# Optimization experiments

Hardware: AMD Instinct MI355X
Metric: run time of the kernel (lower is better)

The kernel has to match this reference:

```python
import jax, jax.numpy as jnp
import numpy as np
from jax import lax

MSIZE = 64
NREG = 9
POOL_W = 256


def conv2d(x, w, b, stride):
    y = lax.conv_general_dilated(x, w, (stride, stride), ((1, 1), (1, 1)),
                                 dimension_numbers=('NCHW', 'OIHW', 'NCHW'))
    return y + b[None, :, None, None]


def resize_nearest(m, h, w):
    # nearest-neighbor resize of a 2D integer mask (matches cv2 INTER_NEAREST floor mapping)
    H, W = m.shape
    ri = (np.arange(h) * H) // h
    ci = (np.arange(w) * W) // w
    return m[ri][:, ci]


def adaptive_max_1d(x, out_size):
    # x: (c, N) -> (c, out_size), torch AdaptiveMaxPool semantics along last dim
    N = x.shape[1]
    j = np.arange(out_size)
    starts = (j * N) // out_size
    ends = -((-(j + 1) * N) // out_size)  # ceil((j+1)*N/out)
    maxlen = int((ends - starts).max())
    idx = starts[:, None] + np.arange(maxlen)[None, :]  # (out, maxlen)
    valid = idx < ends[:, None]
    idx = np.minimum(idx, N - 1)
    g = x[:, idx]  # (c, out, maxlen)
    g = jnp.where(valid[None, :, :], g, -jnp.inf)
    return g.max(axis=2)


def image_cnn(x, masks_np, w1, b1, w2, b2, w3, b3, fcw, fcb):
    f = jax.nn.relu(conv2d(x, w1, b1, 2))
    f = jax.nn.relu(conv2d(f, w2, b2, 2))
    f = conv2d(f, w3, b3, 2)
    _, c, h, w = f.shape
    ff = f.reshape(c, h * w)
    mats = {}
    for i in range(NREG):
        m = resize_nearest(masks_np[i, 0], h, w).reshape(-1)
        if int((m == 1).sum()) >= 10:
            idx = np.nonzero(m == 1)[0]
            pooled = adaptive_max_1d(ff[:, idx], POOL_W)  # (16, 256)
            mats[i] = fcw @ pooled.reshape(-1) + fcb      # (MSIZE*MSIZE,)
    return mats


def mul_forward(cF, sF, content, style, cmasks_np, smasks_np,
                compress_w, compress_b, unzip_w, unzip_b, sp, cp):
    sb, sc, sh, sw = sF.shape
    X = jnp.einsum('oc,bchw->bohw', compress_w, cF) + compress_b[None, :, None, None]
    cb, cc, ch, cw = X.shape
    X = X.reshape(cc, ch * cw)
    X = X - X.mean(axis=1, keepdims=True)
    sM = image_cnn(style, smasks_np, *sp)
    cM = image_cnn(content, cmasks_np, *cp)
    sFF = sF.reshape(sc, sh * sw)
    trans = X
    fmean = jnp.zeros((sc, ch * cw), dtype=cF.dtype)
    for i in range(NREG):
        cm = resize_nearest(cmasks_np[i, 0], ch, cw).reshape(-1)
        sm = resize_nearest(smasks_np[i, 0], sh, sw).reshape(-1)
        if int((cm == 1).sum()) >= 10 and int((sm == 1).sum()) >= 10 and i in sM and i in cM:
            fgc = np.nonzero(cm == 1)[0]
            fgs = np.nonzero(sm == 1)[0]
            sMean = sFF[:, fgs].mean(axis=1, keepdims=True)            # (sc, 1)
            T = sM[i].reshape(MSIZE, MSIZE) @ cM[i].reshape(MSIZE, MSIZE)
            trans = trans.at[:, fgc].set(T @ X[:, fgc])                 # gather-mm-scatter
            fmean = fmean.at[:, fgc].set(jnp.broadcast_to(sMean, (sc, fgc.size)))
    out = jnp.einsum('oc,bchw->bohw', unzip_w, trans.reshape(cb, cc, ch, cw)) \
          + unzip_b[None, :, None, None]
    return out + fmean.reshape(out.shape)


def setup_inputs():
    key = jax.random.key(0)
    ks = jax.random.split(key, 32)
    p = lambda k, s: jax.random.normal(k, s, dtype=jnp.float32) * 0.05
    inp = {}
    inp['cF'] = jax.random.normal(ks[0], (1, 256, 256, 256), dtype=jnp.float32)
    inp['sF'] = jax.random.normal(ks[1], (1, 256, 256, 256), dtype=jnp.float32)
    inp['content'] = jax.random.normal(ks[2], (1, 3, 1024, 1024), dtype=jnp.float32)
    inp['style'] = jax.random.normal(ks[3], (1, 3, 1024, 1024), dtype=jnp.float32)
    inp['cmasks'] = jax.random.randint(ks[4], (9, 1, 256, 256), 0, 2, dtype=jnp.int32)
    inp['smasks'] = jax.random.randint(ks[5], (9, 1, 256, 256), 0, 2, dtype=jnp.int32)
    inp['compress_w'] = p(ks[6], (MSIZE, 256))
    inp['compress_b'] = p(ks[7], (MSIZE,))
    inp['unzip_w'] = p(ks[8], (256, MSIZE))
    inp['unzip_b'] = p(ks[9], (256,))
    for pre, off in (('s', 10), ('c', 20)):
        inp[pre + '_w1'] = p(ks[off + 0], (64, 3, 3, 3))
        inp[pre + '_b1'] = p(ks[off + 1], (64,))
        inp[pre + '_w2'] = p(ks[off + 2], (32, 64, 3, 3))
        inp[pre + '_b2'] = p(ks[off + 3], (32,))
        inp[pre + '_w3'] = p(ks[off + 4], (16, 32, 3, 3))
        inp[pre + '_b3'] = p(ks[off + 5], (16,))
        inp[pre + '_fcw'] = p(ks[off + 6], (MSIZE * MSIZE, 16 * POOL_W))
        inp[pre + '_fcb'] = p(ks[off + 7], (MSIZE * MSIZE,))
    return inp


def reference(cF, sF, content, style, cmasks, smasks,
              compress_w, compress_b, unzip_w, unzip_b,
              s_w1, s_b1, s_w2, s_b2, s_w3, s_b3, s_fcw, s_fcb,
              c_w1, c_b1, c_w2, c_b2, c_w3, c_b3, c_fcw, c_fcb):
    cm_np = np.asarray(cmasks)
    sm_np = np.asarray(smasks)
    sp = (s_w1, s_b1, s_w2, s_b2, s_w3, s_b3, s_fcw, s_fcb)
    cp = (c_w1, c_b1, c_w2, c_b2, c_w3, c_b3, c_fcw, c_fcb)
    return mul_forward(cF, sF, content, style, cm_np, sm_np,
                       compress_w, compress_b, unzip_w, unzip_b, sp, cp)
```

## Files before the change

### kernel.cpp

```cpp
#include <hip/hip_runtime.h>
#include <math.h>

#define TPB 256
constexpr int YC_STRIDE = 68096;

constexpr size_t OFF_COUNTS   = 0x000000;
constexpr size_t OFF_ACTIVE   = 0x000100;
constexpr size_t OFF_LCNT     = 0x000140;
constexpr size_t OFF_RBASE    = 0x000180;
constexpr size_t OFF_MUSUM    = 0x000200;
constexpr size_t OFF_MU       = 0x000400;
constexpr size_t OFF_SSUM     = 0x000800;
constexpr size_t OFF_SMEAN    = 0x00A000;
constexpr size_t OFF_W1T      = 0x00D000;
constexpr size_t OFF_W3T      = 0x00F000;
constexpr size_t OFF_W2T      = 0x014000;
constexpr size_t OFF_CWT      = 0x028000;
constexpr size_t OFF_POOLED   = 0x040000;
constexpr size_t OFF_M        = 0x090000;
constexpr size_t OFF_P        = 0x0E0000;
constexpr size_t OFF_U        = 0x180000;
constexpr size_t OFF_V        = 0x228000;
constexpr size_t OFF_CBITS    = 0x230000;
constexpr size_t OFF_SBITS    = 0x270000;
constexpr size_t OFF_CBITS128 = 0x2B0000;
constexpr size_t OFF_SBITS128 = 0x2C0000;
constexpr size_t OFF_IDX      = 0x2D0000;
constexpr size_t OFF_BC       = 0x3F8000;
constexpr size_t OFF_BBASE    = 0x400000;
constexpr size_t OFF_RLIST    = 0x410000;
constexpr size_t OFF_INV      = 0x460000;
constexpr size_t OFF_XCT      = 0x700000;
constexpr size_t OFF_F1       = 0x1700000;
constexpr size_t OFF_F2       = 0x5700000;
constexpr size_t OFF_F3       = 0x5F00000;
constexpr size_t OFF_YC       = OFF_F1;

__global__ void init_k(int* p, int n) {
    for (int i = blockIdx.x * TPB + threadIdx.x; i < n; i += gridDim.x * TPB) p[i] = 0;
}

__global__ void bits_k(const int* __restrict__ cm, const int* __restrict__ sm,
                       int* __restrict__ cbits, int* __restrict__ sbits, int* __restrict__ counts) {
    int p = blockIdx.x * TPB + threadIdx.x;
    int cb = 0, sb = 0;
#pragma unroll
    for (int r = 0; r < 9; ++r) {
        cb |= (cm[r * 65536 + p] == 1) << r;
        sb |= (sm[r * 65536 + p] == 1) << r;
    }
    cbits[p] = cb; sbits[p] = sb;
    int lane = threadIdx.x & 63;
#pragma unroll
    for (int r = 0; r < 9; ++r) {
        unsigned long long b1 = __ballot((cb >> r) & 1);
        if (lane == 0) atomicAdd(&counts[0 + r], __popcll(b1));
        unsigned long long b2 = __ballot((sb >> r) & 1);
        if (lane == 0) atomicAdd(&counts[16 + r], __popcll(b2));
    }
}

__global__ void bits128_k(const int* __restrict__ cm, const int* __restrict__ sm,
                          int* __restrict__ cbits128, int* __restrict__ sbits128, int* __restrict__ counts) {
    int p = blockIdx.x * TPB + threadIdx.x;
    int y = p >> 7, x = p & 127;
    int src = (2 * y) * 256 + 2 * x;
    int cb = 0, sb = 0;
#pragma unroll
    for (int r = 0; r < 9; ++r) {
        cb |= (cm[r * 65536 + src] == 1) << r;
        sb |= (sm[r * 65536 + src] == 1) << r;
    }
    cbits128[p] = cb; sbits128[p] = sb;
    int lane = threadIdx.x & 63;
#pragma unroll
    for (int r = 0; r < 9; ++r) {
        unsigned long long b1 = __ballot((cb >> r) & 1);
        if (lane == 0) atomicAdd(&counts[32 + r], __popcll(b1));
        unsigned long long b2 = __ballot((sb >> r) & 1);
        if (lane == 0) atomicAdd(&counts[48 + r], __popcll(b2));
    }
}

__global__ void compact_k(const int* __restrict__ sbits128, const int* __restrict__ cbits128,
                          int* __restrict__ idxlist) {
    int r = blockIdx.x, side = blockIdx.y;
    const int* bits = side ? cbits128 : sbits128;
    int* outp = idxlist + (side * 9 + r) * 16384;
    __shared__ int wcnt[4];
    __shared__ int base_s;
    int t = threadIdx.x, w = t >> 6, lane = t & 63;
    if (t == 0) base_s = 0;
    __syncthreads();
    for (int chunk = 0; chunk < 64; ++chunk) {
        int pid = chunk * 256 + t;
        int flag = (bits[pid] >> r) & 1;
        unsigned long long m = __ballot(flag);
        if (lane == 0) wcnt[w] = __popcll(m);
        __syncthreads();
        int base = base_s;
        int woff = 0;
        for (int w2 = 0; w2 < w; ++w2) woff += wcnt[w2];
        if (flag) outp[base + woff + __popcll(m & ((1ull << lane) - 1ull))] = pid;
        __syncthreads();
        if (t == 0) base_s = base + wcnt[0] + wcnt[1] + wcnt[2] + wcnt[3];
    }
}

__global__ void wtr_k(const float* __restrict__ w, float* __restrict__ wT, int OC, int ICK) {
    int i = blockIdx.x * TPB + threadIdx.x;
    int n = OC * ICK;
    if (i < n) {
        int oc = i / ICK;
        int t = i - oc * ICK;
        wT[t * OC + oc] = w[i];
    }
}

__global__ void smean_k(const float* __restrict__ sF, const int* __restrict__ sbits,
                        float* __restrict__ ssump) {
    int c = blockIdx.x;
    int pg = blockIdx.y;
    int t = threadIdx.x;
    float acc[9];
#pragma unroll
    for (int r = 0; r < 9; ++r) acc[r] = 0.f;
    int p0 = pg * 16384;
    for (int p = p0 + t; p < p0 + 16384; p += TPB) {
        float v = sF[c * 65536 + p];
        int b = sbits[p];
#pragma unroll
        for (int r = 0; r < 9; ++r)
            if (b & (1 << r)) acc[r] += v;
    }
    __shared__ float red[9 * TPB];
#pragma unroll
    for (int r = 0; r < 9; ++r) red[r * TPB + t] = acc[r];
    __syncthreads();
    for (int off = TPB / 2; off > 0; off >>= 1) {
        if (t < off)
#pragma unroll
            for (int r = 0; r < 9; ++r) red[r * TPB + t] += red[r * TPB + t + off];
        __syncthreads();
    }
    if (t < 9) ssump[(pg * 9 + t) * 256 + c] = red[t * TPB];
}

__global__ void finalize_k(const int* __restrict__ counts, int* __restrict__ activemask,
                           const float* __restrict__ ssump, float* __restrict__ sMeanArr) {
    __shared__ int am;
    if (threadIdx.x == 0) am = 0;
    __syncthreads();
    if (threadIdx.x < 9) {
        int r = threadIdx.x;
        if (counts[0 + r] >= 10 && counts[16 + r] >= 10 && counts[32 + r] >= 10 && counts[48 + r] >= 10)
            atomicOr(&am, 1 << r);
    }
    __syncthreads();
    if (threadIdx.x == 0) *activemask = am;
    for (int e = threadIdx.x; e < 2560; e += TPB) {
        int r = e >> 8, c = e & 255;
        float v = 0.f;
        if (r < 9 && ((am >> r) & 1)) {
            float s = ssump[(0 * 9 + r) * 256 + c] + ssump[(1 * 9 + r) * 256 + c]
                    + ssump[(2 * 9 + r) * 256 + c] + ssump[(3 * 9 + r) * 256 + c];
            v = s / (float)counts[16 + r];
        }
        sMeanArr[e] = v;
    }
}

__global__ void hist_k(const int* __restrict__ cbits, const int* __restrict__ activemask,
                       int* __restrict__ rmap, int* __restrict__ bc) {
    int b = blockIdx.x, t = threadIdx.x;
    int p = b * 256 + t;
    int am = *activemask;
    int bits = cbits[p] & am;
    int r = bits ? (31 - __clz(bits)) : 9;
    rmap[p] = r;
    __shared__ int wc[4][10];
    int w = t >> 6, lane = t & 63;
#pragma unroll
    for (int rr = 0; rr < 10; ++rr) {
        unsigned long long m = __ballot(r == rr);
        if (lane == rr) wc[w][rr] = __popcll(m);
    }
    __syncthreads();
    if (t < 10) bc[b * 10 + t] = wc[0][t] + wc[1][t] + wc[2][t] + wc[3][t];
}

__global__ void scan_k(const int* __restrict__ bc, int* __restrict__ bbase,
                       int* __restrict__ lcnt, int* __restrict__ rbase) {
    __shared__ int tot[10], Bs[16];
    int t = threadIdx.x;
    if (t < 10) {
        int s = 0;
        for (int b = 0; b < 256; ++b) s += bc[b * 10 + t];
        tot[t] = s;
    }
    __syncthreads();
    if (t == 0) {
        int run = 0;
        for (int r = 0; r < 10; ++r) { Bs[r] = run; run += (tot[r] + 255) & ~255; }
    }
    __syncthreads();
    if (t < 10) {
        lcnt[t] = tot[t];
        rbase[t] = Bs[t];
        int run = Bs[t];
        for (int b = 0; b < 256; ++b) { bbase[b * 10 + t] = run; run += bc[b * 10 + t]; }
    }
}

__global__ void rank_k(const int* __restrict__ rmap, const int* __restrict__ bbase,
                       int* __restrict__ inv, int* __restrict__ rlist) {
    int b = blockIdx.x, t = threadIdx.x;
    int p = b * 256 + t;
    int r = rmap[p];
    __shared__ int wc[4][10];
    int w = t >> 6, lane = t & 63;
    int prefix = 0;
#pragma unroll
    for (int rr = 0; rr < 10; ++rr) {
        unsigned long long m = __ballot(r == rr);
        if (rr == r) prefix = __popcll(m & ((1ull << lane) - 1ull));
        if (lane == rr) wc[w][rr] = __popcll(m);
    }
    __syncthreads();
    int woff = 0;
    for (int w2 = 0; w2 < w; ++w2) woff += wc[w2][r];
    int g = bbase[b * 10 + r] + woff + prefix;
    inv[p] = g;
    rlist[g] = p;
}

__global__ void conv1_k(const float* __restrict__ in, const float* __restrict__ wT,
                        const float* __restrict__ b, float* __restrict__ out) {
    int oy = blockIdx.x >> 1;
    int X0 = (blockIdx.x & 1) << 8;
    int og = blockIdx.y;
    int t = threadIdx.x;
    __shared__ float ev[3][3][260];
    __shared__ float od[3][3][264];
    for (int u = t; u < 1152; u += 256) {
        int ic = u / 384;
        int rem = u - ic * 384;
        int row = rem >> 7, q = rem & 127;
        int iy = 2 * oy - 1 + row;
        float4 v = make_float4(0.f, 0.f, 0.f, 0.f);
        if ((unsigned)iy < 1024u)
            v = *(const float4*)(in + ic * 1048576 + iy * 1024 + 2 * X0 + 4 * q);
        ev[ic][row][2 * q]     = v.x;
        od[ic][row][2 * q + 1] = v.y;
        ev[ic][row][2 * q + 1] = v.z;
        od[ic][row][2 * q + 2] = v.w;
    }
    if (t < 9) {
        int ic = t / 3, row = t % 3;
        int iy = 2 * oy - 1 + row;
        int ix = 2 * X0 - 1;
        float v = 0.f;
        if ((unsigned)iy < 1024u && ix >= 0) v = in[ic * 1048576 + iy * 1024 + ix];
        od[ic][row][0] = v;
    }
    __syncthreads();
    float acc[32];
#pragma unroll
    for (int oc = 0; oc < 32; ++oc) acc[oc] = b[og * 32 + oc];
#pragma unroll
    for (int ic = 0; ic < 3; ++ic)
#pragma unroll
        for (int ky = 0; ky < 3; ++ky) {
            float v0 = od[ic][ky][t];
            float v1 = ev[ic][ky][t];
            float v2 = od[ic][ky][t + 1];
#pragma unroll
            for (int kx = 0; kx < 3; ++kx) {
                float v = kx == 0 ? v0 : (kx == 1 ? v1 : v2);
                const float4* wp = (const float4*)(wT + (ic * 9 + ky * 3 + kx) * 64 + og * 32);
#pragma unroll
                for (int q = 0; q < 8; ++q) {
                    float4 w4 = wp[q];
                    acc[q * 4 + 0] = fmaf(w4.x, v, acc[q * 4 + 0]);
                    acc[q * 4 + 1] = fmaf(w4.y, v, acc[q * 4 + 1]);
                    acc[q * 4 + 2] = fmaf(w4.z, v, acc[q * 4 + 2]);
                    acc[q * 4 + 3] = fmaf(w4.w, v, acc[q * 4 + 3]);
                }
            }
        }
    int idx = oy * 512 + X0 + t;
#pragma unroll
    for (int oc = 0; oc < 32; ++oc) out[(og * 32 + oc) * 262144 + idx] = fmaxf(acc[oc], 0.f);
}

__global__ void f2init_k(const float* __restrict__ b, float* __restrict__ F2) {
    int idx = blockIdx.x * TPB + threadIdx.x;
#pragma unroll
    for (int oc = 0; oc < 32; ++oc) F2[oc * 65536 + idx] = b[oc];
}

__device__ __forceinline__ void c2_load(const float* __restrict__ base, int oy, int t,
                                        float4& r0, float4& r1) {
    int row0 = t >> 7, q0 = t & 127;
    int iy0 = 2 * oy - 1 + row0;
    r0 = make_float4(0.f, 0.f, 0.f, 0.f);
    if ((unsigned)iy0 < 512u) r0 = *(const float4*)(base + iy0 * 512 + 4 * q0);
    r1 = make_float4(0.f, 0.f, 0.f, 0.f);
    if (t < 128) {
        int iy1 = 2 * oy + 1;
        r1 = *(const float4*)(base + iy1 * 512 + 4 * t);
    }
}

__device__ __forceinline__ void c2_store(float (*ev)[260], float (*od)[264], int t,
                                         float4 r0, float4 r1) {
    int row0 = t >> 7, q0 = t & 127;
    ev[row0][2 * q0]     = r0.x;
    od[row0][2 * q0 + 1] = r0.y;
    ev[row0][2 * q0 + 1] = r0.z;
    od[row0][2 * q0 + 2] = r0.w;
    if (t < 128) {
        ev[2][2 * t]     = r1.x;
        od[2][2 * t + 1] = r1.y;
        ev[2][2 * t + 1] = r1.z;
        od[2][2 * t + 2] = r1.w;
    }
}

__device__ __forceinline__ void c2_compute(const float* __restrict__ wT, int ic,
                                           const float (*ev)[260], const float (*od)[264],
                                           int t, float* acc) {
#pragma unroll
    for (int ky = 0; ky < 3; ++ky) {
        float v0 = od[ky][t];
        float v1 = ev[ky][t];
        float v2 = od[ky][t + 1];
#pragma unroll
        for (int kx = 0; kx < 3; ++kx) {
            float v = kx == 0 ? v0 : (kx == 1 ? v1 : v2);
            const float4* wp = (const float4*)(wT + (ic * 9 + ky * 3 + kx) * 32);
#pragma unroll
            for (int q = 0; q < 8; ++q) {
                float4 w4 = wp[q];
                acc[q * 4 + 0] = fmaf(w4.x, v, acc[q * 4 + 0]);
                acc[q * 4 + 1] = fmaf(w4.y, v, acc[q * 4 + 1]);
                acc[q * 4 + 2] = fmaf(w4.z, v, acc[q * 4 + 2]);
                acc[q * 4 + 3] = fmaf(w4.w, v, acc[q * 4 + 3]);
            }
        }
    }
}

__global__ void conv2p_k(const float* __restrict__ in, const float* __restrict__ wT,
                         float* __restrict__ F2) {
    int oy = blockIdx.x;
    int icg = blockIdx.y;
    int t = threadIdx.x;
    __shared__ float ev[2][3][260];
    __shared__ float od[2][3][264];
    if (t < 6) od[t / 3][t % 3][0] = 0.f;
    float acc[32];
#pragma unroll
    for (int oc = 0; oc < 32; ++oc) acc[oc] = 0.f;
    int ic0 = icg * 16;
    float4 r0, r1;
    c2_load(in + ic0 * 262144, oy, t, r0, r1);
    c2_store(ev[0], od[0], t, r0, r1);
    __syncthreads();
#pragma unroll 1
    for (int i = 0; i < 16; i += 2) {
        c2_load(in + (ic0 + i + 1) * 262144, oy, t, r0, r1);
        c2_compute(wT, ic0 + i, ev[0], od[0], t, acc);
        c2_store(ev[1], od[1], t, r0, r1);
        __syncthreads();
        if (i + 2 < 16) c2_load(in + (ic0 + i + 2) * 262144, oy, t, r0, r1);
        c2_compute(wT, ic0 + i + 1, ev[1], od[1], t, acc);
        if (i + 2 < 16) c2_store(ev[0], od[0], t, r0, r1);
        __syncthreads();
    }
    int idx = oy * 256 + t;
#pragma unroll
    for (int oc = 0; oc < 32; ++oc) atomicAdd(&F2[oc * 65536 + idx], acc[oc]);
}

__global__ void relu2_k(float* __restrict__ F2) {
    int i = blockIdx.x * TPB + threadIdx.x;
    float4* p = (float4*)F2;
    float4 v = p[i];
    v.x = fmaxf(v.x, 0.f); v.y = fmaxf(v.y, 0.f);
    v.z = fmaxf(v.z, 0.f); v.w = fmaxf(v.w, 0.f);
    p[i] = v;
}

__global__ void f3init_k(const float* __restrict__ b, float* __restrict__ F3) {
    int idx = blockIdx.x * TPB + threadIdx.x;
#pragma unroll
    for (int oc = 0; oc < 16; ++oc) F3[oc * 16384 + idx] = b[oc];
}

__global__ void conv3p_k(const float* __restrict__ in, const float* __restrict__ wT,
                         float* __restrict__ F3) {
    int idx = blockIdx.x * TPB + threadIdx.x;
    int icg = blockIdx.y;
    int ox = idx & 127, oy = idx >> 7;
    float acc[16];
#pragma unroll
    for (int oc = 0; oc < 16; ++oc) acc[oc] = 0.f;
    for (int ic = icg * 8; ic < icg * 8 + 8; ++ic) {
        const float* base = in + ic * 65536;
#pragma unroll
        for (int ky = 0; ky < 3; ++ky) {
            int iy = 2 * oy - 1 + ky;
            if ((unsigned)iy < 256u)
#pragma unroll
                for (int kx = 0; kx < 3; ++kx) {
                    int ix = 2 * ox - 1 + kx;
                    if ((unsigned)ix < 256u) {
                        float v = base[iy * 256 + ix];
                        const float4* wp = (const float4*)(wT + (ic * 9 + ky * 3 + kx) * 16);
#pragma unroll
                        for (int q = 0; q < 4; ++q) {
                            float4 w4 = wp[q];
                            acc[q * 4 + 0] = fmaf(w4.x, v, acc[q * 4 + 0]);
                            acc[q * 4 + 1] = fmaf(w4.y, v, acc[q * 4 + 1]);
                            acc[q * 4 + 2] = fmaf(w4.z, v, acc[q * 4 + 2]);
                            acc[q * 4 + 3] = fmaf(w4.w, v, acc[q * 4 + 3]);
                        }
                    }
                }
        }
    }
#pragma unroll
    for (int oc = 0; oc < 16; ++oc) atomicAdd(&F3[oc * 16384 + idx], acc[oc]);
}

__global__ void pool_k(const float* __restrict__ f3, const int* __restrict__ idxbase,
                       const int* __restrict__ cnt, float* __restrict__ pooled) {
    int r = blockIdx.x >> 4;
    int c = blockIdx.x & 15;
    int j = threadIdx.x;
    int n = cnt[r];
    float m = 0.f;
    if (n >= 1) {
        int start = (j * n) >> 8;
        int end = ((j + 1) * n + 255) >> 8;
        const int* il = idxbase + r * 16384;
        m = -__builtin_inff();
        for (int t = start; t < end; ++t) m = fmaxf(m, f3[c * 16384 + il[t]]);
    }
    pooled[(r * 16 + c) * 256 + j] = m;
}

__global__ void fc_k(const float* __restrict__ fcw_s, const float* __restrict__ fcb_s,
                     const float* __restrict__ fcw_c, const float* __restrict__ fcb_c,
                     const float* __restrict__ pooled, float* __restrict__ Mout) {
    int row = blockIdx.x;
    int side = blockIdx.y;
    const float* fcw = side ? fcw_c : fcw_s;
    const float* fcb = side ? fcb_c : fcb_s;
    const float* P = pooled + side * 9 * 4096;
    int t = threadIdx.x;
    float acc[9];
#pragma unroll
    for (int r = 0; r < 9; ++r) acc[r] = 0.f;
    for (int k = t; k < 4096; k += TPB) {
        float w = fcw[row * 4096 + k];
#pragma unroll
        for (int r = 0; r < 9; ++r) acc[r] = fmaf(w, P[r * 4096 + k], acc[r]);
    }
    __shared__ float red[9 * TPB];
#pragma unroll
    for (int r = 0; r < 9; ++r) red[r * TPB + t] = acc[r];
    __syncthreads();
    for (int off = TPB / 2; off > 0; off >>= 1) {
        if (t < off)
#pragma unroll
            for (int r = 0; r < 9; ++r) red[r * TPB + t] += red[r * TPB + t + off];
        __syncthreads();
    }
    if (t < 9) Mout[(side * 9 + t) * 4096 + row] = red[t * TPB] + fcb[row];
}

__global__ void xgemm_k(const float* __restrict__ cF, const float* __restrict__ cwT,
                        float* __restrict__ XcT) {
    int p = blockIdx.x * TPB + threadIdx.x;
    int m0 = blockIdx.y * 16;
    float acc[16];
#pragma unroll
    for (int m = 0; m < 16; ++m) acc[m] = 0.f;
    for (int k0 = 0; k0 < 256; k0 += 4) {
        float xv[4];
#pragma unroll
        for (int i = 0; i < 4; ++i) xv[i] = cF[(k0 + i) * 65536 + p];
#pragma unroll
        for (int i = 0; i < 4; ++i) {
            const float4* wp = (const float4*)(cwT + (k0 + i) * 64 + m0);
#pragma unroll
            for (int q = 0; q < 4; ++q) {
                float4 w4 = wp[q];
                acc[q * 4 + 0] = fmaf(w4.x, xv[i], acc[q * 4 + 0]);
                acc[q * 4 + 1] = fmaf(w4.y, xv[i], acc[q * 4 + 1]);
                acc[q * 4 + 2] = fmaf(w4.z, xv[i], acc[q * 4 + 2]);
                acc[q * 4 + 3] = fmaf(w4.w, xv[i], acc[q * 4 + 3]);
            }
        }
    }
    float4* op = (float4*)(XcT + p * 64 + m0);
#pragma unroll
    for (int q = 0; q < 4; ++q)
        op[q] = make_float4(acc[q * 4 + 0], acc[q * 4 + 1], acc[q * 4 + 2], acc[q * 4 + 3]);
}

__global__ void muacc_k(const float* __restrict__ XcT, float* __restrict__ musum) {
    int t = threadIdx.x;
    int m = t & 63, sub = t >> 6;
    int p0 = blockIdx.x * 256;
    float a = 0.f;
    for (int i = 0; i < 64; ++i) a += XcT[(p0 + sub + i * 4) * 64 + m];
    __shared__ float red[TPB];
    red[t] = a;
    __syncthreads();
    if (t < 64) atomicAdd(&musum[t], red[t] + red[t + 64] + red[t + 128] + red[t + 192]);
}

__global__ void mufin_k(const float* __restrict__ musum, float* __restrict__ mu) {
    int t = threadIdx.x;
    if (t < 64) mu[t] = musum[t] * (1.f / 65536.f);
}

__global__ void uprep1_k(const float* __restrict__ uw, const float* __restrict__ M,
                         float* __restrict__ P) {
    int idx = blockIdx.x * TPB + threadIdx.x;
    int r = idx / 16384;
    int rem = idx & 16383;
    int c = rem >> 6, k = rem & 63;
    float a = 0.f;
#pragma unroll 8
    for (int i = 0; i < 64; ++i) a = fmaf(uw[c * 64 + i], M[r * 4096 + i * 64 + k], a);
    P[idx] = a;
}

__global__ void uprep2_k(const float* __restrict__ uw, const float* __restrict__ M,
                         const float* __restrict__ P, float* __restrict__ U) {
    int idx = blockIdx.x * TPB + threadIdx.x;
    int r = idx / 16384;
    int rem = idx & 16383;
    int c = rem >> 6, j = rem & 63;
    if (r == 9) { U[idx] = uw[c * 64 + j]; return; }
    float a = 0.f;
#pragma unroll 8
    for (int k = 0; k < 64; ++k) a = fmaf(P[r * 16384 + c * 64 + k], M[(9 + r) * 4096 + k * 64 + j], a);
    U[idx] = a;
}

__global__ void uprep3_k(const float* __restrict__ U, const float* __restrict__ mu,
                         const float* __restrict__ uzb, const float* __restrict__ sMeanArr,
                         float* __restrict__ V) {
    int r = blockIdx.x;
    int c = threadIdx.x;
    float a = uzb[c] + sMeanArr[r * 256 + c];
#pragma unroll 8
    for (int j = 0; j < 64; ++j) a -= U[r * 16384 + c * 64 + j] * mu[j];
    V[r * 256 + c] = a;
}

__global__ void ygemm_k(const float* __restrict__ XcT, const float* __restrict__ U,
                        const float* __restrict__ V, const int* __restrict__ lcnt,
                        const int* __restrict__ rbase, const int* __restrict__ rlist,
                        float* __restrict__ Yc) {
    int r = blockIdx.x >> 8;
    int c = blockIdx.x & 255;
    int ocg = blockIdx.y;
    int n = lcnt[r];
    int start = c * 256;
    if (start >= n) return;
    int i = start + threadIdx.x;
    bool valid = i < n;
    int gi = rbase[r] + (valid ? i : n - 1);
    int pix = rlist[gi];
    float4 xv[16];
    const float4* xp = (const float4*)(XcT + (size_t)pix * 64);
#pragma unroll
    for (int q = 0; q < 16; ++q) xv[q] = xp[q];
    const float* Ur = U + r * 16384 + ocg * 4096;
    const float* Vr = V + r * 256 + ocg * 64;
#pragma unroll 4
    for (int oc = 0; oc < 64; ++oc) {
        float a = Vr[oc];
        const float4* up = (const float4*)(Ur + oc * 64);
#pragma unroll
        for (int q = 0; q < 16; ++q) {
            float4 u4 = up[q];
            a = fmaf(u4.x, xv[q].x, a);
            a = fmaf(u4.y, xv[q].y, a);
            a = fmaf(u4.z, xv[q].z, a);
            a = fmaf(u4.w, xv[q].w, a);
        }
        if (valid) Yc[(size_t)(ocg * 64 + oc) * YC_STRIDE + gi] = a;
    }
}

__global__ void merge_k(const float* __restrict__ Yc, const int* __restrict__ inv,
                        float* __restrict__ out) {
    int p = blockIdx.x * TPB + threadIdx.x;
    int oc0 = blockIdx.y * 4;
    int gi = inv[p];
#pragma unroll
    for (int j = 0; j < 4; ++j)
        out[(size_t)(oc0 + j) * 65536 + p] = Yc[(size_t)(oc0 + j) * YC_STRIDE + gi];
}

extern "C" void kernel_launch(void* const* d_in, const int* in_sizes, int n_in,
                              void* d_out, int out_size, void* d_ws, size_t ws_size,
                              hipStream_t stream) {
    const float* cF         = (const float*)d_in[0];
    const float* sF         = (const float*)d_in[1];
    const float* content    = (const float*)d_in[2];
    const float* style      = (const float*)d_in[3];
    const int*   cmasks     = (const int*)d_in[4];
    const int*   smasks     = (const int*)d_in[5];
    const float* compress_w = (const float*)d_in[6];
    const float* unzip_w    = (const float*)d_in[8];
    const float* unzip_b    = (const float*)d_in[9];
    const float* s_w1 = (const float*)d_in[10]; const float* s_b1 = (const float*)d_in[11];
    const float* s_w2 = (const float*)d_in[12]; const float* s_b2 = (const float*)d_in[13];
    const float* s_w3 = (const float*)d_in[14]; const float* s_b3 = (const float*)d_in[15];
    const float* s_fcw = (const float*)d_in[16]; const float* s_fcb = (const float*)d_in[17];
    const float* c_w1 = (const float*)d_in[18]; const float* c_b1 = (const float*)d_in[19];
    const float* c_w2 = (const float*)d_in[20]; const float* c_b2 = (const float*)d_in[21];
    const float* c_w3 = (const float*)d_in[22]; const float* c_b3 = (const float*)d_in[23];
    const float* c_fcw = (const float*)d_in[24]; const float* c_fcb = (const float*)d_in[25];
    float* out = (float*)d_out;
    char* ws = (char*)d_ws;
#define WF(o) ((float*)(ws + (o)))
#define WI(o) ((int*)(ws + (o)))

    init_k<<<1, TPB, 0, stream>>>(WI(0), 256);
    bits_k<<<256, TPB, 0, stream>>>(cmasks, smasks, WI(OFF_CBITS), WI(OFF_SBITS), WI(OFF_COUNTS));
    bits128_k<<<64, TPB, 0, stream>>>(cmasks, smasks, WI(OFF_CBITS128), WI(OFF_SBITS128), WI(OFF_COUNTS));
    compact_k<<<dim3(9, 2), TPB, 0, stream>>>(WI(OFF_SBITS128), WI(OFF_CBITS128), WI(OFF_IDX));
    smean_k<<<dim3(256, 4), TPB, 0, stream>>>(sF, WI(OFF_SBITS), WF(OFF_SSUM));
    finalize_k<<<1, TPB, 0, stream>>>(WI(OFF_COUNTS), WI(OFF_ACTIVE), WF(OFF_SSUM), WF(OFF_SMEAN));

    hist_k<<<256, TPB, 0, stream>>>(WI(OFF_CBITS), WI(OFF_ACTIVE), WI(OFF_INV) , WI(OFF_BC));
    scan_k<<<1, TPB, 0, stream>>>(WI(OFF_BC), WI(OFF_BBASE), WI(OFF_LCNT), WI(OFF_RBASE));
    rank_k<<<256, TPB, 0, stream>>>(WI(OFF_INV) , WI(OFF_BBASE), WI(OFF_INV), WI(OFF_RLIST));

    wtr_k<<<64, TPB, 0, stream>>>(compress_w, WF(OFF_CWT), 64, 256);
    xgemm_k<<<dim3(256, 4), TPB, 0, stream>>>(cF, WF(OFF_CWT), WF(OFF_XCT));
    muacc_k<<<256, TPB, 0, stream>>>(WF(OFF_XCT), WF(OFF_MUSUM));
    mufin_k<<<1, 64, 0, stream>>>(WF(OFF_MUSUM), WF(OFF_MU));

    wtr_k<<<7, TPB, 0, stream>>>(s_w1, WF(OFF_W1T), 64, 27);
    wtr_k<<<72, TPB, 0, stream>>>(s_w2, WF(OFF_W2T), 32, 576);
    wtr_k<<<18, TPB, 0, stream>>>(s_w3, WF(OFF_W3T), 16, 288);
    conv1_k<<<dim3(1024, 2), TPB, 0, stream>>>(style, WF(OFF_W1T), s_b1, WF(OFF_F1));
    f2init_k<<<256, TPB, 0, stream>>>(s_b2, WF(OFF_F2));
    conv2p_k<<<dim3(256, 4), TPB, 0, stream>>>(WF(OFF_F1), WF(OFF_W2T), WF(OFF_F2));
    relu2_k<<<2048, TPB, 0, stream>>>(WF(OFF_F2));
    f3init_k<<<64, TPB, 0, stream>>>(s_b3, WF(OFF_F3));
    conv3p_k<<<dim3(64, 4), TPB, 0, stream>>>(WF(OFF_F2), WF(OFF_W3T), WF(OFF_F3));
    pool_k<<<144, TPB, 0, stream>>>(WF(OFF_F3), WI(OFF_IDX), WI(OFF_COUNTS) + 48, WF(OFF_POOLED));

    wtr_k<<<7, TPB, 0, stream>>>(c_w1, WF(OFF_W1T), 64, 27);
    wtr_k<<<72, TPB, 0, stream>>>(c_w2, WF(OFF_W2T), 32, 576);
    wtr_k<<<18, TPB, 0, stream>>>(c_w3, WF(OFF_W3T), 16, 288);
    conv1_k<<<dim3(1024, 2), TPB, 0, stream>>>(content, WF(OFF_W1T), c_b1, WF(OFF_F1));
    f2init_k<<<256, TPB, 0, stream>>>(c_b2, WF(OFF_F2));
    conv2p_k<<<dim3(256, 4), TPB, 0, stream>>>(WF(OFF_F1), WF(OFF_W2T), WF(OFF_F2));
    relu2_k<<<2048, TPB, 0, stream>>>(WF(OFF_F2));
    f3init_k<<<64, TPB, 0, stream>>>(c_b3, WF(OFF_F3));
    conv3p_k<<<dim3(64, 4), TPB, 0, stream>>>(WF(OFF_F2), WF(OFF_W3T), WF(OFF_F3));
    pool_k<<<144, TPB, 0, stream>>>(WF(OFF_F3), WI(OFF_IDX) + 9 * 16384, WI(OFF_COUNTS) + 32,
                                    WF(OFF_POOLED) + 9 * 4096);

    fc_k<<<dim3(4096, 2), TPB, 0, stream>>>(s_fcw, s_fcb, c_fcw, c_fcb, WF(OFF_POOLED), WF(OFF_M));

    uprep1_k<<<576, TPB, 0, stream>>>(unzip_w, WF(OFF_M), WF(OFF_P));
    uprep2_k<<<640, TPB, 0, stream>>>(unzip_w, WF(OFF_M), WF(OFF_P), WF(OFF_U));
    uprep3_k<<<10, TPB, 0, stream>>>(WF(OFF_U), WF(OFF_MU), unzip_b, WF(OFF_SMEAN), WF(OFF_V));

    ygemm_k<<<dim3(2560, 4), TPB, 0, stream>>>(WF(OFF_XCT), WF(OFF_U), WF(OFF_V),
                                               WI(OFF_LCNT), WI(OFF_RBASE), WI(OFF_RLIST), WF(OFF_YC));
    merge_k<<<dim3(256, 64), TPB, 0, stream>>>(WF(OFF_YC), WI(OFF_INV), out);
}
```

Baseline: 1.120 ms.

## Retile conv1 and conv2 threads to 4 pixels by 8 channels

Conv1 and conv2 now give each thread 4 adjacent output pixels and 8 output channels, instead of 1 pixel and 32 channels. Each wave takes its channel group from a wave-uniform readfirstlane index, so weight loads stay scalar and uniform. Shared-memory input reads become float4 vectors that are reused across the 4 pixels, and conv1 writes its output as float4. This cuts LDS and weight-load traffic per FMA. Conv2's atomics become strided scalar atomics across 4 pixels per thread, which may hurt coalescing.

```diff
diff --git a/kernel.cpp b/kernel.cpp
--- a/kernel.cpp
+++ b/kernel.cpp
@@ -234,12 +234,21 @@
     rlist[g] = p;
 }
 
+__device__ __forceinline__ void ld8(float* d, const float* __restrict__ p) {
+    float4 a = *(const float4*)p;
+    float4 b = *(const float4*)(p + 4);
+    d[0] = a.x; d[1] = a.y; d[2] = a.z; d[3] = a.w;
+    d[4] = b.x; d[5] = b.y; d[6] = b.z; d[7] = b.w;
+}
+
 __global__ void conv1_k(const float* __restrict__ in, const float* __restrict__ wT,
                         const float* __restrict__ b, float* __restrict__ out) {
     int oy = blockIdx.x >> 1;
     int X0 = (blockIdx.x & 1) << 8;
-    int og = blockIdx.y;
+    int og32 = blockIdx.y;
     int t = threadIdx.x;
+    int g = t & 63;
+    int og = __builtin_amdgcn_readfirstlane(t >> 6);
     __shared__ float ev[3][3][260];
     __shared__ float od[3][3][264];
     for (int u = t; u < 1152; u += 256) {
@@ -264,33 +273,43 @@
         od[ic][row][0] = v;
     }
     __syncthreads();
-    float acc[32];
-#pragma unroll
-    for (int oc = 0; oc < 32; ++oc) acc[oc] = b[og * 32 + oc];
+    int ocb = og32 * 32 + og * 8;
+    float bias[8];
+    ld8(bias, b + ocb);
+    float acc[4][8];
+#pragma unroll
+    for (int j = 0; j < 4; ++j)
+#pragma unroll
+        for (int c = 0; c < 8; ++c) acc[j][c] = bias[c];
 #pragma unroll
     for (int ic = 0; ic < 3; ++ic)
 #pragma unroll
         for (int ky = 0; ky < 3; ++ky) {
-            float v0 = od[ic][ky][t];
-            float v1 = ev[ic][ky][t];
-            float v2 = od[ic][ky][t + 1];
-#pragma unroll
-            for (int kx = 0; kx < 3; ++kx) {
-                float v = kx == 0 ? v0 : (kx == 1 ? v1 : v2);
-                const float4* wp = (const float4*)(wT + (ic * 9 + ky * 3 + kx) * 64 + og * 32);
-#pragma unroll
-                for (int q = 0; q < 8; ++q) {
-                    float4 w4 = wp[q];
-                    acc[q * 4 + 0] = fmaf(w4.x, v, acc[q * 4 + 0]);
-                    acc[q * 4 + 1] = fmaf(w4.y, v, acc[q * 4 + 1]);
-                    acc[q * 4 + 2] = fmaf(w4.z, v, acc[q * 4 + 2]);
-                    acc[q * 4 + 3] = fmaf(w4.w, v, acc[q * 4 + 3]);
-                }
+            float4 e4 = *(const float4*)&ev[ic][ky][4 * g];
+            float4 o4 = *(const float4*)&od[ic][ky][4 * g];
+            float  o5 = od[ic][ky][4 * g + 4];
+            float e_[4] = {e4.x, e4.y, e4.z, e4.w};
+            float o_[5] = {o4.x, o4.y, o4.z, o4.w, o5};
+            const float* wbase = wT + (ic * 9 + ky * 3) * 64 + ocb;
+            float wA[8], wB[8], wC[8];
+            ld8(wA, wbase);
+            ld8(wB, wbase + 64);
+            ld8(wC, wbase + 128);
+#pragma unroll
+            for (int j = 0; j < 4; ++j) {
+                float v0 = o_[j], v1 = e_[j], v2 = o_[j + 1];
+#pragma unroll
+                for (int c = 0; c < 8; ++c)
+                    acc[j][c] = fmaf(wA[c], v0, fmaf(wB[c], v1, fmaf(wC[c], v2, acc[j][c])));
             }
         }
-    int idx = oy * 512 + X0 + t;
-#pragma unroll
-    for (int oc = 0; oc < 32; ++oc) out[(og * 32 + oc) * 262144 + idx] = fmaxf(acc[oc], 0.f);
+    int idx = oy * 512 + X0 + 4 * g;
+#pragma unroll
+    for (int c = 0; c < 8; ++c) {
+        float4 o = make_float4(fmaxf(acc[0][c], 0.f), fmaxf(acc[1][c], 0.f),
+                               fmaxf(acc[2][c], 0.f), fmaxf(acc[3][c], 0.f));
+        *(float4*)(out + (size_t)(ocb + c) * 262144 + idx) = o;
+    }
 }
 
 __global__ void f2init_k(const float* __restrict__ b, float* __restrict__ F2) {
@@ -329,24 +348,25 @@
 
 __device__ __forceinline__ void c2_compute(const float* __restrict__ wT, int ic,
                                            const float (*ev)[260], const float (*od)[264],
-                                           int t, float* acc) {
+                                           int g, int og, float (*acc)[8]) {
 #pragma unroll
     for (int ky = 0; ky < 3; ++ky) {
-        float v0 = od[ky][t];
-        float v1 = ev[ky][t];
-        float v2 = od[ky][t + 1];
-#pragma unroll
-        for (int kx = 0; kx < 3; ++kx) {
-            float v = kx == 0 ? v0 : (kx == 1 ? v1 : v2);
-            const float4* wp = (const float4*)(wT + (ic * 9 + ky * 3 + kx) * 32);
-#pragma unroll
-            for (int q = 0; q < 8; ++q) {
-                float4 w4 = wp[q];
-                acc[q * 4 + 0] = fmaf(w4.x, v, acc[q * 4 + 0]);
-                acc[q * 4 + 1] = fmaf(w4.y, v, acc[q * 4 + 1]);
-                acc[q * 4 + 2] = fmaf(w4.z, v, acc[q * 4 + 2]);
-                acc[q * 4 + 3] = fmaf(w4.w, v, acc[q * 4 + 3]);
-            }
+        float4 e4 = *(const float4*)&ev[ky][4 * g];
+        float4 o4 = *(const float4*)&od[ky][4 * g];
+        float  o5 = od[ky][4 * g + 4];
+        float e_[4] = {e4.x, e4.y, e4.z, e4.w};
+        float o_[5] = {o4.x, o4.y, o4.z, o4.w, o5};
+        const float* wbase = wT + (ic * 9 + ky * 3) * 32 + og * 8;
+        float wA[8], wB[8], wC[8];
+        ld8(wA, wbase);
+        ld8(wB, wbase + 32);
+        ld8(wC, wbase + 64);
+#pragma unroll
+        for (int j = 0; j < 4; ++j) {
+            float v0 = o_[j], v1 = e_[j], v2 = o_[j + 1];
+#pragma unroll
+            for (int c = 0; c < 8; ++c)
+                acc[j][c] = fmaf(wA[c], v0, fmaf(wB[c], v1, fmaf(wC[c], v2, acc[j][c])));
         }
     }
 }
@@ -356,12 +376,16 @@
     int oy = blockIdx.x;
     int icg = blockIdx.y;
     int t = threadIdx.x;
+    int g = t & 63;
+    int og = __builtin_amdgcn_readfirstlane(t >> 6);
     __shared__ float ev[2][3][260];
     __shared__ float od[2][3][264];
     if (t < 6) od[t / 3][t % 3][0] = 0.f;
-    float acc[32];
-#pragma unroll
-    for (int oc = 0; oc < 32; ++oc) acc[oc] = 0.f;
+    float acc[4][8];
+#pragma unroll
+    for (int j = 0; j < 4; ++j)
+#pragma unroll
+        for (int c = 0; c < 8; ++c) acc[j][c] = 0.f;
     int ic0 = icg * 16;
     float4 r0, r1;
     c2_load(in + ic0 * 262144, oy, t, r0, r1);
@@ -370,17 +394,20 @@
 #pragma unroll 1
     for (int i = 0; i < 16; i += 2) {
         c2_load(in + (ic0 + i + 1) * 262144, oy, t, r0, r1);
-        c2_compute(wT, ic0 + i, ev[0], od[0], t, acc);
+        c2_compute(wT, ic0 + i, ev[0], od[0], g, og, acc);
         c2_store(ev[1], od[1], t, r0, r1);
         __syncthreads();
         if (i + 2 < 16) c2_load(in + (ic0 + i + 2) * 262144, oy, t, r0, r1);
-        c2_compute(wT, ic0 + i + 1, ev[1], od[1], t, acc);
+        c2_compute(wT, ic0 + i + 1, ev[1], od[1], g, og, acc);
         if (i + 2 < 16) c2_store(ev[0], od[0], t, r0, r1);
         __syncthreads();
     }
-    int idx = oy * 256 + t;
-#pragma unroll
-    for (int oc = 0; oc < 32; ++oc) atomicAdd(&F2[oc * 65536 + idx], acc[oc]);
+    int base = oy * 256 + 4 * g;
+#pragma unroll
+    for (int c = 0; c < 8; ++c)
+#pragma unroll
+        for (int j = 0; j < 4; ++j)
+            atomicAdd(&F2[(og * 8 + c) * 65536 + base + j], acc[j][c]);
 }
 
 __global__ void relu2_k(float* __restrict__ F2) {
```

After: 1.162 ms. +3.8%, slower.
